# Kernel tuning notes

Hardware: AMD Instinct MI355X
Metric: run time of the kernel (lower is better)

Reference implementation:

```python
import jax, jax.numpy as jnp
import numpy as np

B, S, D = 2, 4096, 2048
H = 16
DN, DR = 128, 64          # qk_nope_head_dim, qk_rope_head_dim
DQK = DN + DR             # 192
DV = 128                  # v_head_dim
QL, KVL = 512, 512        # q_lora_rank, kv_lora_rank
L = 64                    # block_len
SCALE = DQK ** -0.5
ROPE_THETA = 10000.0


def rms_norm(x, w, eps=1e-6):
    x = x.astype(jnp.float32)
    return x * jax.lax.rsqrt(jnp.mean(x * x, axis=-1, keepdims=True) + eps) * w


def apply_rope(x, cos, sin):
    # x: [b, s, h, d]; cos/sin: [s, d//2]; pairs are consecutive (view(-1,2))
    shp = x.shape
    x2 = x.reshape(shp[:-1] + (-1, 2))
    xr, xi = x2[..., 0], x2[..., 1]
    c = cos[None, :, None, :]
    s_ = sin[None, :, None, :]
    yr = xr * c - xi * s_
    yi = xr * s_ + xi * c
    return jnp.stack([yr, yi], axis=-1).reshape(shp)


def ssa(q, k, v, init_state):
    # chunked causal linear attention; q,k: [b,s,h,dk], v: [b,s,h,dv]
    b, s, h, dk = q.shape
    dv = v.shape[-1]
    nc = s // L
    qc = q.reshape(b, nc, L, h, dk)
    kc = k.reshape(b, nc, L, h, dk)
    vc = v.reshape(b, nc, L, h, dv)
    # per-chunk k^T v outer products -> [b,c,h,dk,dv]
    kv = jnp.einsum('bclhk,bclhv->bchkv', kc, vc)
    cs = jnp.cumsum(kv, axis=1)
    # exclusive prefix (state at chunk start) + initial state
    states = jnp.concatenate([jnp.zeros_like(cs[:, :1]), cs[:, :-1]], axis=1) + init_state[:, None]
    inter = jnp.einsum('bclhk,bchkv->bclhv', qc, states)
    sc = jnp.einsum('bclhk,bcmhk->bchlm', qc, kc)
    mask = jnp.tril(jnp.ones((L, L), dtype=bool))
    sc = jnp.where(mask, sc, 0.0)
    intra = jnp.einsum('bchlm,bcmhv->bclhv', sc, vc)
    return (inter + intra).reshape(b, s, h, dv)


def setup_inputs() -> dict:
    key = jax.random.key(0)
    ks = jax.random.split(key, 8)
    x = jax.random.normal(ks[0], (B, S, D), dtype=jnp.float32)
    # rope tables for qk_rope_head_dim
    inv = 1.0 / (ROPE_THETA ** (np.arange(0, DR, 2, dtype=np.float32) / DR))
    ang = np.outer(np.arange(S, dtype=np.float32), inv)
    cos = jnp.asarray(np.cos(ang), dtype=jnp.float32)
    sin = jnp.asarray(np.sin(ang), dtype=jnp.float32)
    std = 0.02
    wq_a = jax.random.normal(ks[1], (QL, D), dtype=jnp.float32) * std
    wq_b = jax.random.normal(ks[2], (H * DQK, QL), dtype=jnp.float32) * std
    wkv_a = jax.random.normal(ks[3], (KVL + DR, D), dtype=jnp.float32) * std
    wkv_b = jax.random.normal(ks[4], (H * (DN + DV), KVL), dtype=jnp.float32) * std
    wo = jax.random.normal(ks[5], (D, H * DV), dtype=jnp.float32) * std
    q_norm_w = jnp.ones((QL,), dtype=jnp.float32)
    kv_norm_w = jnp.ones((KVL,), dtype=jnp.float32)
    init_state = jnp.zeros((B, H, DQK, DV), dtype=jnp.float32)
    return {"x": x, "start_pos": 0, "cos": cos, "sin": sin,
            "wq_a": wq_a, "wq_b": wq_b, "wkv_a": wkv_a, "wkv_b": wkv_b,
            "wo": wo, "q_norm_w": q_norm_w, "kv_norm_w": kv_norm_w,
            "init_state": init_state}


def reference(x, start_pos, cos, sin, wq_a, wq_b, wkv_a, wkv_b, wo,
              q_norm_w, kv_norm_w, init_state):
    b, s, _ = x.shape
    q = rms_norm(x @ wq_a.T, q_norm_w) @ wq_b.T
    q = q.reshape(b, s, H, DQK)
    q_nope, q_pe = q[..., :DN], q[..., DN:]
    q_pe = apply_rope(q_pe, cos, sin)
    kvp = x @ wkv_a.T
    kv_lat, k_pe = kvp[..., :KVL], kvp[..., KVL:]
    k_pe = apply_rope(k_pe[:, :, None, :], cos, sin)  # [b,s,1,DR]
    kv = rms_norm(kv_lat, kv_norm_w) @ wkv_b.T
    kv = kv.reshape(b, s, H, DN + DV)
    k_nope, v = kv[..., :DN], kv[..., DN:]
    q = jnp.concatenate([q_nope, q_pe], axis=-1)
    k = jnp.concatenate([k_nope, jnp.broadcast_to(k_pe, (b, s, H, DR))], axis=-1)
    q = jax.nn.elu(q) + 1.0
    k = jax.nn.elu(k) + 1.0
    out = ssa(q, k, v, init_state) * SCALE
    out = out.reshape(b, s, H * DV) @ wo.T
    return out
```

## Files before the change

kernel.cpp:

```cpp
#include <hip/hip_runtime.h>

static __device__ __align__(256) unsigned char g_ws[645200000];

typedef __attribute__((ext_vector_type(8))) __bf16 bf16x8;
typedef __attribute__((ext_vector_type(4))) float  f32x4;
typedef __attribute__((ext_vector_type(8))) unsigned short u16x8;

__device__ __forceinline__ short f2bf(float f) {
    union { float f; unsigned u; } v; v.f = f;
    unsigned r = v.u + 0x7FFFu + ((v.u >> 16) & 1u);
    return (short)(r >> 16);
}
__device__ __forceinline__ float bf2f(unsigned short u) {
    union { unsigned u; float f; } v; v.u = ((unsigned)u) << 16;
    return v.f;
}
__device__ __forceinline__ float elu1(float x) {
    return x > 0.f ? x + 1.f : __expf(x);
}
__device__ __forceinline__ void gload_lds16(const void* g, void* l) {
    __builtin_amdgcn_global_load_lds(
        (const __attribute__((address_space(1))) unsigned int*)g,
        (__attribute__((address_space(3))) unsigned int*)l, 16, 0, 0);
}

#define MFMA16(a, b, c) __builtin_amdgcn_mfma_f32_16x16x32_bf16((a), (b), (c), 0, 0, 0)

__global__ __launch_bounds__(256) void cvt_bf16(
    const float* __restrict__ src, short* __restrict__ dst, int n)
{
    const int i = (blockIdx.x * 256 + threadIdx.x) * 4;
    if (i < n) {
        const float4 v = *(const float4*)(src + i);
        ushort4 o;
        o.x = (unsigned short)f2bf(v.x);
        o.y = (unsigned short)f2bf(v.y);
        o.z = (unsigned short)f2bf(v.z);
        o.w = (unsigned short)f2bf(v.w);
        *(ushort4*)(dst + i) = o;
    }
}

template <int OUT_BF16>
__global__ __launch_bounds__(256) void gemm_lds(
    const short* __restrict__ A, int lda,
    const short* __restrict__ Bt, int ldb,
    void* __restrict__ Cv, int ldc,
    int Nvalid, int K)
{
    __shared__ short As[128 * 32];
    __shared__ short Bs[128 * 32];
    const int row0 = blockIdx.x * 128;
    const int col0 = blockIdx.y * 128;
    const int t = threadIdx.x;
    const int lane = t & 63;
    const int wave = t >> 6;
    const int wr = (wave >> 1) * 64;
    const int wc = (wave & 1) * 64;
    const int l15 = lane & 15;
    const int kg = (lane >> 4) * 8;
    const int rbase = (lane >> 4) * 4;

    const int srow = (lane >> 2);
    const int sbyte = (lane & 3) * 16;

    f32x4 acc[4][4];
#pragma unroll
    for (int i = 0; i < 4; ++i)
#pragma unroll
        for (int j = 0; j < 4; ++j) acc[i][j] = (f32x4){0.f, 0.f, 0.f, 0.f};

    const char* aBase = (const char*)A + ((size_t)(row0 + wave * 32 + srow) * lda) * 2 + sbyte;
    const char* bBase = (const char*)Bt + ((size_t)(col0 + wave * 32 + srow) * ldb) * 2 + sbyte;
    const size_t aRow16 = (size_t)lda * 32;
    const size_t bRow16 = (size_t)ldb * 32;

    for (int k0 = 0; k0 < K; k0 += 32) {
        const size_t kb = (size_t)k0 * 2;
        gload_lds16(aBase + kb,          &As[(wave * 32) * 32]);
        gload_lds16(aBase + kb + aRow16, &As[(wave * 32 + 16) * 32]);
        gload_lds16(bBase + kb,          &Bs[(wave * 32) * 32]);
        gload_lds16(bBase + kb + bRow16, &Bs[(wave * 32 + 16) * 32]);
        __syncthreads();
        bf16x8 af[4], bfr[4];
#pragma unroll
        for (int i = 0; i < 4; ++i) af[i] = *(const bf16x8*)&As[(wr + i * 16 + l15) * 32 + kg];
#pragma unroll
        for (int j = 0; j < 4; ++j) bfr[j] = *(const bf16x8*)&Bs[(wc + j * 16 + l15) * 32 + kg];
#pragma unroll
        for (int i = 0; i < 4; ++i)
#pragma unroll
            for (int j = 0; j < 4; ++j)
                acc[i][j] = MFMA16(af[i], bfr[j], acc[i][j]);
        __syncthreads();
    }
#pragma unroll
    for (int i = 0; i < 4; ++i) {
#pragma unroll
        for (int j = 0; j < 4; ++j) {
            const int cc = col0 + wc + j * 16 + l15;
            if (cc < Nvalid) {
#pragma unroll
                for (int q = 0; q < 4; ++q) {
                    const size_t off = (size_t)(row0 + wr + i * 16 + rbase + q) * ldc + cc;
                    if (OUT_BF16) ((short*)Cv)[off] = f2bf(acc[i][j][q]);
                    else          ((float*)Cv)[off] = acc[i][j][q];
                }
            }
        }
    }
}

__global__ __launch_bounds__(256) void rms_rope(
    const short* __restrict__ Y1,
    const float* __restrict__ qw, const float* __restrict__ kvw,
    const float* __restrict__ cosT, const float* __restrict__ sinT,
    short* __restrict__ qn, short* __restrict__ kvn, float* __restrict__ kpe)
{
    __shared__ float red[256];
    const int row = blockIdx.x;
    const int s = row & 4095;
    const int t = threadIdx.x;
    const unsigned short* yr = (const unsigned short*)(Y1 + (size_t)row * 1088);

    float v0 = bf2f(yr[t]), v1 = bf2f(yr[t + 256]);
    red[t] = v0 * v0 + v1 * v1;
    __syncthreads();
    for (int off = 128; off > 0; off >>= 1) {
        if (t < off) red[t] += red[t + off];
        __syncthreads();
    }
    float rs = rsqrtf(red[0] / 512.f + 1e-6f);
    __syncthreads();
    qn[(size_t)row * 512 + t]       = f2bf(v0 * rs * qw[t]);
    qn[(size_t)row * 512 + t + 256] = f2bf(v1 * rs * qw[t + 256]);

    float u0 = bf2f(yr[512 + t]), u1 = bf2f(yr[768 + t]);
    red[t] = u0 * u0 + u1 * u1;
    __syncthreads();
    for (int off = 128; off > 0; off >>= 1) {
        if (t < off) red[t] += red[t + off];
        __syncthreads();
    }
    float rs2 = rsqrtf(red[0] / 512.f + 1e-6f);
    kvn[(size_t)row * 512 + t]       = f2bf(u0 * rs2 * kvw[t]);
    kvn[(size_t)row * 512 + t + 256] = f2bf(u1 * rs2 * kvw[t + 256]);

    if (t < 32) {
        float xr = bf2f(yr[1024 + 2 * t]), xi = bf2f(yr[1024 + 2 * t + 1]);
        float cc = cosT[(size_t)s * 32 + t], sn = sinT[(size_t)s * 32 + t];
        kpe[(size_t)row * 64 + 2 * t]     = xr * cc - xi * sn;
        kpe[(size_t)row * 64 + 2 * t + 1] = xr * sn + xi * cc;
    }
}

__global__ __launch_bounds__(192) void build_q(
    const short* __restrict__ qbig,
    const float* __restrict__ cosT, const float* __restrict__ sinT,
    short* __restrict__ q_ssa)
{
    const int row = blockIdx.x;
    const int s = row & 4095;
    const int b = row >> 12;
    const int d = threadIdx.x;
    const unsigned short* qr = (const unsigned short*)(qbig + (size_t)row * 3072);
#pragma unroll 1
    for (int h = 0; h < 16; ++h) {
        float val;
        if (d < 128) {
            val = bf2f(qr[h * 192 + d]);
        } else {
            const int p = (d - 128) >> 1;
            const float xr = bf2f(qr[h * 192 + 128 + 2 * p]);
            const float xi = bf2f(qr[h * 192 + 128 + 2 * p + 1]);
            const float cc = cosT[(size_t)s * 32 + p];
            const float sn = sinT[(size_t)s * 32 + p];
            val = ((d & 1) == 0) ? (xr * cc - xi * sn) : (xr * sn + xi * cc);
        }
        val = elu1(val);
        q_ssa[((size_t)(b * 16 + h) * 4096 + s) * 192 + d] = f2bf(val);
    }
}

__global__ __launch_bounds__(256) void build_kv(
    const short* __restrict__ kvbig, const float* __restrict__ kpe,
    short* __restrict__ k_ssa, short* __restrict__ v_ssa)
{
    const int row = blockIdx.x;
    const int s = row & 4095;
    const int b = row >> 12;
    const int t = threadIdx.x;
    const unsigned short* kr = (const unsigned short*)(kvbig + (size_t)row * 4096);
    const float* pe = kpe + (size_t)row * 64;
#pragma unroll 1
    for (int h = 0; h < 16; ++h) {
        const size_t kbase = ((size_t)(b * 16 + h) * 4096 + s) * 192;
        const size_t vbase = ((size_t)(b * 16 + h) * 4096 + s) * 128;
        if (t < 128) {
            k_ssa[kbase + t] = f2bf(elu1(bf2f(kr[h * 256 + t])));
            v_ssa[vbase + t] = (short)kr[h * 256 + 128 + t];
        } else if (t < 192) {
            const int d = t - 128;
            k_ssa[kbase + 128 + d] = f2bf(elu1(pe[d]));
        }
    }
}

__global__ __launch_bounds__(256) void init_t_kern(
    const float* __restrict__ init, float* __restrict__ initT)
{
    __shared__ float tile[32][33];
    const int bh = blockIdx.y;
    const int tk = blockIdx.x % 6, tv = blockIdx.x / 6;
    const int r0 = threadIdx.x >> 5, c = threadIdx.x & 31;
    const float* src = init + (size_t)bh * 24576;
    float* dst = initT + (size_t)bh * 24576;
#pragma unroll
    for (int p = 0; p < 4; ++p) {
        const int rr = r0 + 8 * p;
        tile[rr][c] = src[(size_t)(tk * 32 + rr) * 128 + tv * 32 + c];
    }
    __syncthreads();
#pragma unroll
    for (int p = 0; p < 4; ++p) {
        const int rr = r0 + 8 * p;
        dst[(size_t)(tv * 32 + rr) * 192 + tk * 32 + c] = tile[c][rr];
    }
}

__global__ __launch_bounds__(256, 3) void ssa_kv(
    const short* __restrict__ k_ssa, const short* __restrict__ v_ssa,
    short* __restrict__ kvcT)
{
    __shared__ short smem[25600];
    short (*lkt)[72] = (short(*)[72])smem;
    short (*lvt)[72] = (short(*)[72])(smem + 192 * 72);
    short (*outT)[200] = (short(*)[200])smem;
    const int c = blockIdx.x, h = blockIdx.y, b = blockIdx.z;
    const int bh = b * 16 + h;
    const short* Kc = k_ssa + ((size_t)bh * 4096 + c * 64) * 192;
    const short* Vc = v_ssa + ((size_t)bh * 4096 + c * 64) * 128;
    const int t = threadIdx.x, lane = t & 63, w = t >> 6;
    const int l15 = lane & 15, kg = (lane >> 4) * 8, rbase = (lane >> 4) * 4;

    for (int i = t; i < 64 * 48; i += 256) {
        const int row = i / 48, c4 = (i % 48) * 4;
        ushort4 kv4 = *(const ushort4*)(Kc + (size_t)row * 192 + c4);
        lkt[c4 + 0][row] = (short)kv4.x;
        lkt[c4 + 1][row] = (short)kv4.y;
        lkt[c4 + 2][row] = (short)kv4.z;
        lkt[c4 + 3][row] = (short)kv4.w;
    }
    for (int i = t; i < 64 * 32; i += 256) {
        const int row = i >> 5, c4 = (i & 31) * 4;
        ushort4 vv = *(const ushort4*)(Vc + (size_t)row * 128 + c4);
        lvt[c4 + 0][row] = (short)vv.x;
        lvt[c4 + 1][row] = (short)vv.y;
        lvt[c4 + 2][row] = (short)vv.z;
        lvt[c4 + 3][row] = (short)vv.w;
    }
    __syncthreads();

    f32x4 acc[2][12];
#pragma unroll
    for (int i = 0; i < 2; ++i)
#pragma unroll
        for (int j = 0; j < 12; ++j) acc[i][j] = (f32x4){0.f, 0.f, 0.f, 0.f};
#pragma unroll
    for (int ks = 0; ks < 2; ++ks) {
        bf16x8 af[2];
#pragma unroll
        for (int i = 0; i < 2; ++i) af[i] = *(const bf16x8*)&lvt[w * 32 + i * 16 + l15][ks * 32 + kg];
#pragma unroll
        for (int j = 0; j < 12; ++j) {
            const bf16x8 bk = *(const bf16x8*)&lkt[j * 16 + l15][ks * 32 + kg];
#pragma unroll
            for (int i = 0; i < 2; ++i) acc[i][j] = MFMA16(af[i], bk, acc[i][j]);
        }
    }
    __syncthreads();
#pragma unroll
    for (int i = 0; i < 2; ++i)
#pragma unroll
        for (int j = 0; j < 12; ++j)
#pragma unroll
            for (int q = 0; q < 4; ++q)
                outT[w * 32 + i * 16 + rbase + q][j * 16 + l15] = f2bf(acc[i][j][q]);
    __syncthreads();

    short* kvp = kvcT + ((size_t)bh * 64 + c) * 24576;
    for (int i = t; i < 3072; i += 256) {
        const int s8 = i * 8;
        const int row = s8 / 192, col = s8 % 192;
        *(u16x8*)(kvp + s8) = *(const u16x8*)&outT[row][col];
    }
}

__global__ __launch_bounds__(256) void ssa_scan(
    short* __restrict__ kvc, const float* __restrict__ initT)
{
    const int bh = blockIdx.y;
    const int e8 = (blockIdx.x * 256 + threadIdx.x) * 8;
    float st[8];
    {
        const float4 i0 = *(const float4*)(initT + (size_t)bh * 24576 + e8);
        const float4 i1 = *(const float4*)(initT + (size_t)bh * 24576 + e8 + 4);
        st[0] = i0.x; st[1] = i0.y; st[2] = i0.z; st[3] = i0.w;
        st[4] = i1.x; st[5] = i1.y; st[6] = i1.z; st[7] = i1.w;
    }
    short* p = kvc + (size_t)bh * 64 * 24576 + e8;
    for (int cc = 0; cc < 64; ++cc) {
        const u16x8 v = *(const u16x8*)p;
        u16x8 o;
#pragma unroll
        for (int j = 0; j < 8; ++j) o[j] = (unsigned short)f2bf(st[j]);
        *(u16x8*)p = o;
#pragma unroll
        for (int j = 0; j < 8; ++j) st[j] += bf2f(v[j]);
        p += 24576;
    }
}

__global__ __launch_bounds__(256, 2) void ssa_out(
    const short* __restrict__ q_ssa, const short* __restrict__ k_ssa,
    const short* __restrict__ v_ssa, const short* __restrict__ states,
    short* __restrict__ attnb)
{
    __shared__ short lk[64][200];
    __shared__ short lvt[128][72];
    __shared__ short lst[128][104];
    __shared__ short lsc[64][72];
    const int c = blockIdx.x, h = blockIdx.y, b = blockIdx.z;
    const int bh = b * 16 + h;
    const short* Qb = q_ssa + ((size_t)bh * 4096 + c * 64) * 192;
    const short* Kc = k_ssa + ((size_t)bh * 4096 + c * 64) * 192;
    const short* Vc = v_ssa + ((size_t)bh * 4096 + c * 64) * 128;
    const short* st = states + ((size_t)bh * 64 + c) * 24576;
    const int t = threadIdx.x, lane = t & 63, w = t >> 6;
    const int l15 = lane & 15, kg = (lane >> 4) * 8, rbase = (lane >> 4) * 4;

    bf16x8 aq[6];
    {
        const short* Qr = Qb + (size_t)(w * 16 + l15) * 192 + kg;
#pragma unroll
        for (int ks = 0; ks < 6; ++ks) aq[ks] = *(const bf16x8*)(Qr + ks * 32);
    }
    for (int i = t; i < 1536; i += 256) {
        const int row = i / 24, c8 = (i % 24) * 8;
        *(u16x8*)&lk[row][c8] = *(const u16x8*)(Kc + (size_t)row * 192 + c8);
    }
    for (int i = t; i < 2048; i += 256) {
        const int row = i >> 5, c4 = (i & 31) * 4;
        ushort4 vv = *(const ushort4*)(Vc + (size_t)row * 128 + c4);
        lvt[c4 + 0][row] = (short)vv.x;
        lvt[c4 + 1][row] = (short)vv.y;
        lvt[c4 + 2][row] = (short)vv.z;
        lvt[c4 + 3][row] = (short)vv.w;
    }
    for (int i = t; i < 1536; i += 256) {
        const int row = i / 12, c8 = (i % 12) * 8;
        *(u16x8*)&lst[row][c8] = *(const u16x8*)(st + (size_t)row * 192 + c8);
    }
    __syncthreads();

    {
        f32x4 sc[4];
#pragma unroll
        for (int j = 0; j < 4; ++j) sc[j] = (f32x4){0.f, 0.f, 0.f, 0.f};
#pragma unroll
        for (int ks = 0; ks < 6; ++ks)
#pragma unroll
            for (int j = 0; j < 4; ++j) {
                const bf16x8 bk = *(const bf16x8*)&lk[j * 16 + l15][ks * 32 + kg];
                sc[j] = MFMA16(aq[ks], bk, sc[j]);
            }
#pragma unroll
        for (int j = 0; j < 4; ++j)
#pragma unroll
            for (int q = 0; q < 4; ++q) {
                const int l = w * 16 + rbase + q;
                const int m = j * 16 + l15;
                lsc[l][m] = f2bf((m <= l) ? sc[j][q] : 0.f);
            }
    }
    __syncthreads();

    f32x4 acc[8];
#pragma unroll
    for (int j = 0; j < 8; ++j) acc[j] = (f32x4){0.f, 0.f, 0.f, 0.f};
#pragma unroll
    for (int ks = 0; ks < 2; ++ks) {
        const bf16x8 as = *(const bf16x8*)&lsc[w * 16 + l15][ks * 32 + kg];
#pragma unroll
        for (int j = 0; j < 8; ++j) {
            const bf16x8 bv = *(const bf16x8*)&lvt[j * 16 + l15][ks * 32 + kg];
            acc[j] = MFMA16(as, bv, acc[j]);
        }
    }
#pragma unroll
    for (int ks = 0; ks < 3; ++ks)
#pragma unroll
        for (int j = 0; j < 8; ++j) {
            const bf16x8 bs = *(const bf16x8*)&lst[j * 16 + l15][ks * 32 + kg];
            acc[j] = MFMA16(aq[ks], bs, acc[j]);
        }
    __syncthreads();
    for (int i = t; i < 1536; i += 256) {
        const int row = i / 12, c8 = (i % 12) * 8;
        *(u16x8*)&lst[row][c8] = *(const u16x8*)(st + (size_t)row * 192 + 96 + c8);
    }
    __syncthreads();
#pragma unroll
    for (int ks = 3; ks < 6; ++ks)
#pragma unroll
        for (int j = 0; j < 8; ++j) {
            const bf16x8 bs = *(const bf16x8*)&lst[j * 16 + l15][(ks - 3) * 32 + kg];
            acc[j] = MFMA16(aq[ks], bs, acc[j]);
        }

    const float scale = 0.07216878364870322f;
#pragma unroll
    for (int j = 0; j < 8; ++j)
#pragma unroll
        for (int q = 0; q < 4; ++q) {
            const int l = w * 16 + rbase + q;
            const int dv = j * 16 + l15;
            attnb[((size_t)(b * 4096 + c * 64 + l)) * 2048 + h * 128 + dv] = f2bf(acc[j][q] * scale);
        }
}

extern "C" void kernel_launch(void* const* d_in, const int* in_sizes, int n_in,
                              void* d_out, int out_size, void* d_ws, size_t ws_size,
                              hipStream_t stream) {
    const float* x     = (const float*)d_in[0];
    const float* cosT  = (const float*)d_in[2];
    const float* sinT  = (const float*)d_in[3];
    const float* wq_a  = (const float*)d_in[4];
    const float* wq_b  = (const float*)d_in[5];
    const float* wkv_a = (const float*)d_in[6];
    const float* wkv_b = (const float*)d_in[7];
    const float* wo    = (const float*)d_in[8];
    const float* qw    = (const float*)d_in[9];
    const float* kvw   = (const float*)d_in[10];
    const float* init  = (const float*)d_in[11];
    float* out = (float*)d_out;

    void* base = nullptr;
    hipGetSymbolAddress(&base, HIP_SYMBOL(g_ws));
    char* ws = (char*)base;
    size_t off = 0;
    auto take = [&](size_t bytes) -> char* {
        char* p = ws + off;
        off += (bytes + 255) & ~(size_t)255;
        return p;
    };
    short* xb    = (short*)take((size_t)8192 * 2048 * 2);
    short* wab   = (short*)take((size_t)1152 * 2048 * 2);
    short* wqbb  = (short*)take((size_t)3072 * 512 * 2);
    short* wkvbb = (short*)take((size_t)4096 * 512 * 2);
    short* wob   = (short*)take((size_t)2048 * 2048 * 2);
    short* y1b   = (short*)take((size_t)8192 * 1088 * 2);
    short* qnb   = (short*)take((size_t)8192 * 512 * 2);
    short* kvnb  = (short*)take((size_t)8192 * 512 * 2);
    float* kpe   = (float*)take((size_t)8192 * 64 * 4);
    short* qbig  = (short*)take((size_t)8192 * 3072 * 2);
    short* kvbig = (short*)take((size_t)8192 * 4096 * 2);
    short* qs    = (short*)take((size_t)2 * 16 * 4096 * 192 * 2);
    short* ksb   = (short*)take((size_t)2 * 16 * 4096 * 192 * 2);
    short* vsb   = (short*)take((size_t)2 * 16 * 4096 * 128 * 2);
    short* kvcT  = (short*)take((size_t)2048 * 24576 * 2);
    float* initT = (float*)take((size_t)32 * 24576 * 4);
    short* attnb = (short*)take((size_t)8192 * 2048 * 2);

    cvt_bf16<<<(8192 * 2048 / 4 + 255) / 256, 256, 0, stream>>>(x, xb, 8192 * 2048);
    cvt_bf16<<<(512 * 2048 / 4 + 255) / 256, 256, 0, stream>>>(wq_a, wab, 512 * 2048);
    cvt_bf16<<<(576 * 2048 / 4 + 255) / 256, 256, 0, stream>>>(wkv_a, wab + (size_t)512 * 2048, 576 * 2048);
    hipMemsetAsync(wab + (size_t)1088 * 2048, 0, (size_t)64 * 2048 * 2, stream);
    cvt_bf16<<<(3072 * 512 / 4 + 255) / 256, 256, 0, stream>>>(wq_b, wqbb, 3072 * 512);
    cvt_bf16<<<(4096 * 512 / 4 + 255) / 256, 256, 0, stream>>>(wkv_b, wkvbb, 4096 * 512);
    cvt_bf16<<<(2048 * 2048 / 4 + 255) / 256, 256, 0, stream>>>(wo, wob, 2048 * 2048);
    init_t_kern<<<dim3(24, 32), 256, 0, stream>>>(init, initT);

    gemm_lds<1><<<dim3(64, 9), 256, 0, stream>>>(xb, 2048, wab, 2048, y1b, 1088, 1088, 2048);
    rms_rope<<<8192, 256, 0, stream>>>(y1b, qw, kvw, cosT, sinT, qnb, kvnb, kpe);
    gemm_lds<1><<<dim3(64, 24), 256, 0, stream>>>(qnb, 512, wqbb, 512, qbig, 3072, 3072, 512);
    build_q<<<8192, 192, 0, stream>>>(qbig, cosT, sinT, qs);
    gemm_lds<1><<<dim3(64, 32), 256, 0, stream>>>(kvnb, 512, wkvbb, 512, kvbig, 4096, 4096, 512);
    build_kv<<<8192, 256, 0, stream>>>(kvbig, kpe, ksb, vsb);
    ssa_kv<<<dim3(64, 16, 2), 256, 0, stream>>>(ksb, vsb, kvcT);
    ssa_scan<<<dim3(12, 32), 256, 0, stream>>>(kvcT, initT);
    ssa_out<<<dim3(64, 16, 2), 256, 0, stream>>>(qs, ksb, vsb, kvcT, attnb);
    gemm_lds<0><<<dim3(64, 16), 256, 0, stream>>>(attnb, 2048, wob, 2048, out, 2048, 2048, 2048);
}
```

Baseline: 688.8 us.

## Replace GEMM with 256x256-tile, 4-stage pipelined, swizzled-LDS kernel

Replaces the 128x128 single-buffered GEMM with a 512-thread kernel that computes 256x256 output tiles. It prefetches K-tiles into a 4-deep LDS ring using direct global-to-LDS loads, waits with explicit vmcnt counts, and uses one barrier per iteration instead of two. It also XOR-swizzles the LDS layout to avoid bank conflicts, remaps block IDs for better XCD/L2 locality, and raises wave priority around the MFMAs. The aim is to hide memory latency and increase data reuse in all four projection GEMMs, at the cost of 128KB of LDS, a larger register footprint, and extra zero-padding of the first weight matrix to 1280 rows.

```diff
diff --git a/kernel.cpp b/kernel.cpp
--- a/kernel.cpp
+++ b/kernel.cpp
@@ -42,73 +42,95 @@
 }
 
 template <int OUT_BF16>
-__global__ __launch_bounds__(256) void gemm_lds(
+__global__ __launch_bounds__(512, 2) void gemm256(
     const short* __restrict__ A, int lda,
     const short* __restrict__ Bt, int ldb,
     void* __restrict__ Cv, int ldc,
-    int Nvalid, int K)
-{
-    __shared__ short As[128 * 32];
-    __shared__ short Bs[128 * 32];
-    const int row0 = blockIdx.x * 128;
-    const int col0 = blockIdx.y * 128;
+    int Nvalid, int K, int nbx)
+{
+    __shared__ short lds[65536];
+    char* ldsB = (char*)lds;
     const int t = threadIdx.x;
-    const int lane = t & 63;
-    const int wave = t >> 6;
-    const int wr = (wave >> 1) * 64;
-    const int wc = (wave & 1) * 64;
+    const int lane = t & 63, w = t >> 6;
+
+    const int cpx = gridDim.x >> 3;
+    const int id = (blockIdx.x & 7) * cpx + (blockIdx.x >> 3);
+    const int row0 = (id % nbx) * 256;
+    const int col0 = (id / nbx) * 256;
+
+    const int r_in = lane >> 2;
+    const int sw_src = ((lane & 3) << 4) ^ (((lane >> 4) & 3) << 4);
+    const char* aSrc = (const char*)A + ((size_t)(row0 + w * 32 + r_in) * lda) * 2 + sw_src;
+    const char* bSrc = (const char*)Bt + ((size_t)(col0 + w * 32 + r_in) * ldb) * 2 + sw_src;
+    const size_t aStep = (size_t)lda * 32;
+    const size_t bStep = (size_t)ldb * 32;
+    char* aDst = ldsB + (w * 2) * 1024 + lane * 16;
+    char* bDst = ldsB + 65536 + (w * 2) * 1024 + lane * 16;
+
+    const int wr = (w >> 2) * 128, wc = (w & 3) * 64;
     const int l15 = lane & 15;
-    const int kg = (lane >> 4) * 8;
+    const int kxor = ((lane >> 4) * 16) ^ (((l15 >> 2) & 3) << 4);
+
+    const int NT = K >> 5;
+
+    auto STAGE = [&](int j) {
+        const int sb = (j & 3) * 16384;
+        const size_t kb = (size_t)j * 64;
+        gload_lds16(aSrc + kb,         aDst + sb);
+        gload_lds16(aSrc + kb + aStep, aDst + sb + 1024);
+        gload_lds16(bSrc + kb,         bDst + sb);
+        gload_lds16(bSrc + kb + bStep, bDst + sb + 1024);
+    };
+
+    f32x4 acc[8][4];
+#pragma unroll
+    for (int i = 0; i < 8; ++i)
+#pragma unroll
+        for (int j = 0; j < 4; ++j) acc[i][j] = (f32x4){0.f, 0.f, 0.f, 0.f};
+
+    STAGE(0); STAGE(1); STAGE(2);
+
+#pragma unroll 1
+    for (int kt = 0; kt < NT; ++kt) {
+        if (kt < NT - 2)        asm volatile("s_waitcnt vmcnt(8)" ::: "memory");
+        else if (kt == NT - 2)  asm volatile("s_waitcnt vmcnt(4)" ::: "memory");
+        else                    asm volatile("s_waitcnt vmcnt(0)" ::: "memory");
+        __builtin_amdgcn_s_barrier();
+        __builtin_amdgcn_sched_barrier(0);
+        if (kt + 3 < NT) STAGE(kt + 3);
+        const char* aS = ldsB + (kt & 3) * 16384;
+        const char* bS = ldsB + 65536 + (kt & 3) * 16384;
+        bf16x8 af[8], bf4[4];
+#pragma unroll
+        for (int i = 0; i < 8; ++i)
+            af[i] = *(const bf16x8*)(aS + (wr + i * 16 + l15) * 64 + kxor);
+#pragma unroll
+        for (int j = 0; j < 4; ++j)
+            bf4[j] = *(const bf16x8*)(bS + (wc + j * 16 + l15) * 64 + kxor);
+        __builtin_amdgcn_s_setprio(1);
+#pragma unroll
+        for (int i = 0; i < 8; ++i)
+#pragma unroll
+            for (int j = 0; j < 4; ++j)
+                acc[i][j] = MFMA16(af[i], bf4[j], acc[i][j]);
+        __builtin_amdgcn_s_setprio(0);
+    }
+
     const int rbase = (lane >> 4) * 4;
-
-    const int srow = (lane >> 2);
-    const int sbyte = (lane & 3) * 16;
-
-    f32x4 acc[4][4];
-#pragma unroll
-    for (int i = 0; i < 4; ++i)
-#pragma unroll
-        for (int j = 0; j < 4; ++j) acc[i][j] = (f32x4){0.f, 0.f, 0.f, 0.f};
-
-    const char* aBase = (const char*)A + ((size_t)(row0 + wave * 32 + srow) * lda) * 2 + sbyte;
-    const char* bBase = (const char*)Bt + ((size_t)(col0 + wave * 32 + srow) * ldb) * 2 + sbyte;
-    const size_t aRow16 = (size_t)lda * 32;
-    const size_t bRow16 = (size_t)ldb * 32;
-
-    for (int k0 = 0; k0 < K; k0 += 32) {
-        const size_t kb = (size_t)k0 * 2;
-        gload_lds16(aBase + kb,          &As[(wave * 32) * 32]);
-        gload_lds16(aBase + kb + aRow16, &As[(wave * 32 + 16) * 32]);
-        gload_lds16(bBase + kb,          &Bs[(wave * 32) * 32]);
-        gload_lds16(bBase + kb + bRow16, &Bs[(wave * 32 + 16) * 32]);
-        __syncthreads();
-        bf16x8 af[4], bfr[4];
-#pragma unroll
-        for (int i = 0; i < 4; ++i) af[i] = *(const bf16x8*)&As[(wr + i * 16 + l15) * 32 + kg];
-#pragma unroll
-        for (int j = 0; j < 4; ++j) bfr[j] = *(const bf16x8*)&Bs[(wc + j * 16 + l15) * 32 + kg];
-#pragma unroll
-        for (int i = 0; i < 4; ++i)
-#pragma unroll
-            for (int j = 0; j < 4; ++j)
-                acc[i][j] = MFMA16(af[i], bfr[j], acc[i][j]);
-        __syncthreads();
-    }
-#pragma unroll
-    for (int i = 0; i < 4; ++i) {
+#pragma unroll
+    for (int i = 0; i < 8; ++i)
 #pragma unroll
         for (int j = 0; j < 4; ++j) {
             const int cc = col0 + wc + j * 16 + l15;
             if (cc < Nvalid) {
 #pragma unroll
                 for (int q = 0; q < 4; ++q) {
-                    const size_t off = (size_t)(row0 + wr + i * 16 + rbase + q) * ldc + cc;
-                    if (OUT_BF16) ((short*)Cv)[off] = f2bf(acc[i][j][q]);
-                    else          ((float*)Cv)[off] = acc[i][j][q];
+                    const size_t o = (size_t)(row0 + wr + i * 16 + rbase + q) * ldc + cc;
+                    if (OUT_BF16) ((short*)Cv)[o] = f2bf(acc[i][j][q]);
+                    else          ((float*)Cv)[o] = acc[i][j][q];
                 }
             }
         }
-    }
 }
 
 __global__ __launch_bounds__(256) void rms_rope(
@@ -455,7 +477,7 @@
         return p;
     };
     short* xb    = (short*)take((size_t)8192 * 2048 * 2);
-    short* wab   = (short*)take((size_t)1152 * 2048 * 2);
+    short* wab   = (short*)take((size_t)1280 * 2048 * 2);
     short* wqbb  = (short*)take((size_t)3072 * 512 * 2);
     short* wkvbb = (short*)take((size_t)4096 * 512 * 2);
     short* wob   = (short*)take((size_t)2048 * 2048 * 2);
@@ -475,20 +497,20 @@
     cvt_bf16<<<(8192 * 2048 / 4 + 255) / 256, 256, 0, stream>>>(x, xb, 8192 * 2048);
     cvt_bf16<<<(512 * 2048 / 4 + 255) / 256, 256, 0, stream>>>(wq_a, wab, 512 * 2048);
     cvt_bf16<<<(576 * 2048 / 4 + 255) / 256, 256, 0, stream>>>(wkv_a, wab + (size_t)512 * 2048, 576 * 2048);
-    hipMemsetAsync(wab + (size_t)1088 * 2048, 0, (size_t)64 * 2048 * 2, stream);
+    hipMemsetAsync(wab + (size_t)1088 * 2048, 0, (size_t)192 * 2048 * 2, stream);
     cvt_bf16<<<(3072 * 512 / 4 + 255) / 256, 256, 0, stream>>>(wq_b, wqbb, 3072 * 512);
     cvt_bf16<<<(4096 * 512 / 4 + 255) / 256, 256, 0, stream>>>(wkv_b, wkvbb, 4096 * 512);
     cvt_bf16<<<(2048 * 2048 / 4 + 255) / 256, 256, 0, stream>>>(wo, wob, 2048 * 2048);
     init_t_kern<<<dim3(24, 32), 256, 0, stream>>>(init, initT);
 
-    gemm_lds<1><<<dim3(64, 9), 256, 0, stream>>>(xb, 2048, wab, 2048, y1b, 1088, 1088, 2048);
+    gemm256<1><<<160, 512, 0, stream>>>(xb, 2048, wab, 2048, y1b, 1088, 1088, 2048, 32);
     rms_rope<<<8192, 256, 0, stream>>>(y1b, qw, kvw, cosT, sinT, qnb, kvnb, kpe);
-    gemm_lds<1><<<dim3(64, 24), 256, 0, stream>>>(qnb, 512, wqbb, 512, qbig, 3072, 3072, 512);
+    gemm256<1><<<384, 512, 0, stream>>>(qnb, 512, wqbb, 512, qbig, 3072, 3072, 512, 32);
     build_q<<<8192, 192, 0, stream>>>(qbig, cosT, sinT, qs);
-    gemm_lds<1><<<dim3(64, 32), 256, 0, stream>>>(kvnb, 512, wkvbb, 512, kvbig, 4096, 4096, 512);
+    gemm256<1><<<512, 512, 0, stream>>>(kvnb, 512, wkvbb, 512, kvbig, 4096, 4096, 512, 32);
     build_kv<<<8192, 256, 0, stream>>>(kvbig, kpe, ksb, vsb);
     ssa_kv<<<dim3(64, 16, 2), 256, 0, stream>>>(ksb, vsb, kvcT);
     ssa_scan<<<dim3(12, 32), 256, 0, stream>>>(kvcT, initT);
     ssa_out<<<dim3(64, 16, 2), 256, 0, stream>>>(qs, ksb, vsb, kvcT, attnb);
-    gemm_lds<0><<<dim3(64, 16), 256, 0, stream>>>(attnb, 2048, wob, 2048, out, 2048, 2048, 2048);
-}
+    gemm256<0><<<256, 512, 0, stream>>>(attnb, 2048, wob, 2048, out, 2048, 2048, 2048, 32);
+}
```

Measured after the change: 641.0 us. 6.9% less time.
